# Performance work log

Hardware: AMD Instinct MI355X
Metric: run time of the kernel (lower is better)

Reference implementation:

```python
import jax, jax.numpy as jnp
import numpy as np

K = 39      # num_fields (Criteo)
B = 8192    # batch
D = 64      # embed_dim

def setup_inputs() -> dict:
    key = jax.random.key(0)
    k1, k2 = jax.random.split(key)
    x = jax.random.normal(k1, (K, B, D), dtype=jnp.float32)
    field_cov_weight = jax.random.normal(k2, (K, K), dtype=jnp.float32)
    return {"x": x, "field_cov_weight": field_cov_weight}

def reference(x, field_cov_weight):
    # Symmetrized field interaction matrix S = (W^T + W)/2, [K,K]
    S = 0.5 * (field_cov_weight + field_cov_weight.T)
    # Full weighted pairwise sum: sum_{k,l} S[k,l] * x[k] * x[l]  -> [B,D]
    # (fused; never materializes the [K,K,B,D] outer product the torch code builds)
    full = jnp.einsum('kij,kl,lij->ij', x, S, x)
    # Diagonal terms: sum_k S[k,k] * x[k]^2  -> [B,D]
    diag = jnp.einsum('k,kij->ij', jnp.diagonal(S), x * x)
    # FwFM second order: off-diagonal pairs counted once
    return 0.5 * (full - diag)
```

## Files before the change

### kernel.cpp

```cpp
#include <hip/hip_runtime.h>


#define KF 39
#define NPAIR (KF * (KF - 1) / 2)
#define NELEM (8192 * 64)
#define NV2   (NELEM / 2)

__global__ void fwfm_coef_kernel(const float* __restrict__ W, float* __restrict__ c) {
    const int t = blockIdx.x * 256 + threadIdx.x;
    if (t >= KF * KF) return;
    const int k = t / KF;
    const int l = t - k * KF;
    if (l < k) {
        c[(k * (k - 1)) / 2 + l] = 0.5f * (W[k * KF + l] + W[l * KF + k]);
    }
}

__global__ __attribute__((amdgpu_flat_work_group_size(256, 256), amdgpu_waves_per_eu(4, 5)))
void fwfm_kernel(const float* __restrict__ x,
                 const float* __restrict__ c,
                 float* __restrict__ out) {
    const int n = blockIdx.x * 256 + threadIdx.x;

    const float2* __restrict__ x2 = reinterpret_cast<const float2*>(x);

    float2 v[KF];
#pragma unroll
    for (int k = 0; k < KF; ++k) {
        v[k] = x2[(size_t)k * NV2 + n];
    }

    float accx = 0.0f, accy = 0.0f;
    int p = 0;
#pragma unroll
    for (int k = 1; k < KF; ++k) {
        float wx = 0.0f, wy = 0.0f;
#pragma unroll
        for (int l = 0; l < k; ++l) {
            const float cc = c[p++];
            wx = fmaf(cc, v[l].x, wx);
            wy = fmaf(cc, v[l].y, wy);
        }
        accx = fmaf(v[k].x, wx, accx);
        accy = fmaf(v[k].y, wy, accy);
    }

    float2 o;
    o.x = accx;
    o.y = accy;
    reinterpret_cast<float2*>(out)[n] = o;
}

extern "C" void kernel_launch(void* const* d_in, const int* in_sizes, int n_in,
                              void* d_out, int out_size, void* d_ws, size_t ws_size,
                              hipStream_t stream) {
    const float* x = (const float*)d_in[0];
    const float* W = (const float*)d_in[1];
    float* out = (float*)d_out;
    float* coef = (float*)d_ws;

    fwfm_coef_kernel<<<(KF * KF + 255) / 256, 256, 0, stream>>>(W, coef);
    fwfm_kernel<<<NV2 / 256, 256, 0, stream>>>(x, coef, out);
}
```

Before: 117.1 us.

## Fuse coefficient symmetrization into main kernel via shared memory

Removes the separate coefficient-prep kernel launch. Each block now builds the symmetrized pair coefficients itself into LDS while the x loads are in flight, then reads coefficients from LDS instead of global/scalar memory. This saves a launch and the dependency between two kernels, at the cost of redundant per-block W reads, a __syncthreads, and LDS reads (possibly broadcast) replacing what may have been scalar loads.

```diff
diff --git a/kernel.cpp b/kernel.cpp
--- a/kernel.cpp
+++ b/kernel.cpp
@@ -2,33 +2,50 @@
 
 
 #define KF 39
+#define KK (KF * KF)
 #define NPAIR (KF * (KF - 1) / 2)
 #define NELEM (8192 * 64)
 #define NV2   (NELEM / 2)
-
-__global__ void fwfm_coef_kernel(const float* __restrict__ W, float* __restrict__ c) {
-    const int t = blockIdx.x * 256 + threadIdx.x;
-    if (t >= KF * KF) return;
-    const int k = t / KF;
-    const int l = t - k * KF;
-    if (l < k) {
-        c[(k * (k - 1)) / 2 + l] = 0.5f * (W[k * KF + l] + W[l * KF + k]);
-    }
-}
+#define COEF_ITER 6
 
 __global__ __attribute__((amdgpu_flat_work_group_size(256, 256), amdgpu_waves_per_eu(4, 5)))
 void fwfm_kernel(const float* __restrict__ x,
-                 const float* __restrict__ c,
+                 const float* __restrict__ W,
                  float* __restrict__ out) {
-    const int n = blockIdx.x * 256 + threadIdx.x;
+    const int tid = threadIdx.x;
+    const int n = blockIdx.x * 256 + tid;
 
     const float2* __restrict__ x2 = reinterpret_cast<const float2*>(x);
+
+    __shared__ float cs[NPAIR];
+
+    float wa[COEF_ITER], wb[COEF_ITER];
+    int   off[COEF_ITER];
+#pragma unroll
+    for (int i = 0; i < COEF_ITER; ++i) {
+        const int  t  = tid + i * 256;
+        const bool in = (t < KK);
+        const int  tc = in ? t : 0;
+        const int  k  = tc / KF;
+        const int  l  = tc - k * KF;
+        off[i] = (in && l < k) ? (k * (k - 1)) / 2 + l : -1;
+        wa[i] = W[tc];
+        wb[i] = W[l * KF + k];
+    }
 
     float2 v[KF];
 #pragma unroll
     for (int k = 0; k < KF; ++k) {
         v[k] = x2[(size_t)k * NV2 + n];
     }
+
+#pragma unroll
+    for (int i = 0; i < COEF_ITER; ++i) {
+        if (off[i] >= 0) {
+            cs[off[i]] = 0.5f * (wa[i] + wb[i]);
+        }
+    }
+    __syncthreads();
 
     float accx = 0.0f, accy = 0.0f;
     int p = 0;
@@ -37,7 +54,7 @@
         float wx = 0.0f, wy = 0.0f;
 #pragma unroll
         for (int l = 0; l < k; ++l) {
-            const float cc = c[p++];
+            const float cc = cs[p++];
             wx = fmaf(cc, v[l].x, wx);
             wy = fmaf(cc, v[l].y, wy);
         }
@@ -57,8 +74,7 @@
     const float* x = (const float*)d_in[0];
     const float* W = (const float*)d_in[1];
     float* out = (float*)d_out;
-    float* coef = (float*)d_ws;
+    (void)d_ws; (void)ws_size;
 
-    fwfm_coef_kernel<<<(KF * KF + 255) / 256, 256, 0, stream>>>(W, coef);
-    fwfm_kernel<<<NV2 / 256, 256, 0, stream>>>(x, coef, out);
+    fwfm_kernel<<<NV2 / 256, 256, 0, stream>>>(x, W, out);
 }
```

Result: slower. 120.8 us (+3.1%).
